# Kernel tuning notes

Measured on AMD Instinct MI355X. Metric: run time of the kernel, lower is better.

The kernel has to match this reference:

```python
import jax, jax.numpy as jnp
import numpy as np

D_MODEL = 1024
N_HEADS = 16
D_H = D_MODEL // N_HEADS
MAX_LEN = 2048
BATCH = 2
SEQ = 2048
EPS = 1e-8
W_SCALE = 0.02


def _rms_norm(x, w):
    # RMSNorm: x * rsqrt(mean(x^2) + eps) * w
    ms = jnp.mean(jnp.square(x), axis=-1, keepdims=True)
    return w * (x * jax.lax.rsqrt(ms + EPS))


def setup_inputs() -> dict:
    key = jax.random.key(0)
    ks = jax.random.split(key, 12)
    d = D_MODEL
    inp = {
        "x": jax.random.normal(ks[0], (BATCH, SEQ, d), dtype=jnp.float32),
        "t_bias": jnp.zeros((1,), dtype=jnp.float32),  # unused by the module
        "p_bias": jax.random.normal(ks[1], (MAX_LEN, N_HEADS), dtype=jnp.float32),
        # AMS layer params (Linear stored as [in, out])
        "wq": jax.random.normal(ks[2], (d, d), dtype=jnp.float32) * W_SCALE,
        "bq": jnp.zeros((d,), dtype=jnp.float32),
        "wk": jax.random.normal(ks[3], (d, d), dtype=jnp.float32) * W_SCALE,
        "bk": jnp.zeros((d,), dtype=jnp.float32),
        "wv": jax.random.normal(ks[4], (d, d), dtype=jnp.float32) * W_SCALE,
        "bv": jnp.zeros((d,), dtype=jnp.float32),
        "wu": jax.random.normal(ks[5], (d, d), dtype=jnp.float32) * W_SCALE,
        "bu": jnp.zeros((d,), dtype=jnp.float32),
        "g_ams": jnp.ones((d,), dtype=jnp.float32),   # shared RMSNorm weight in AMSLayer
        # MFFN layer params
        "w0": jax.random.normal(ks[6], (d, d), dtype=jnp.float32) * W_SCALE,
        "b0": jnp.zeros((d,), dtype=jnp.float32),
        "w1": jax.random.normal(ks[7], (d, 2 * d), dtype=jnp.float32) * W_SCALE,
        "b1": jnp.zeros((2 * d,), dtype=jnp.float32),
        "w2": jax.random.normal(ks[8], (d, d), dtype=jnp.float32) * W_SCALE,
        "b2": jnp.zeros((d,), dtype=jnp.float32),
        "g_mffn": jnp.ones((d,), dtype=jnp.float32),
    }
    return inp


def reference(x, t_bias, p_bias, wq, bq, wk, bk, wv, bv, wu, bu, g_ams,
              w0, b0, w1, b1, w2, b2, g_mffn):
    B, S, d = x.shape
    H, dh = N_HEADS, D_H

    # ---- AMS layer ----
    x_norm = _rms_norm(x, g_ams)

    def proj(w, b):
        # [B,S,d] -> [B,H,S,dh]
        return (x_norm @ w + b).reshape(B, S, H, dh).transpose(0, 2, 1, 3)

    q = proj(wq, bq)
    k = proj(wk, bk)
    v = proj(wv, bv)

    scale = 1.0 / np.sqrt(dh).astype(np.float32)
    score = jnp.einsum('bhsd,bhtd->bhst', q, k) * scale
    # additive positional bias: p_bias[:S].T -> [H,S], broadcast over query dim
    score = score + p_bias[:S, :].T[None, :, None, :]

    attn = jax.nn.silu(score)                        # SiLU instead of softmax
    out = jnp.einsum('bhst,bhtd->bhsd', attn, v)
    out = out.transpose(0, 2, 1, 3).reshape(B, S, d)

    u = jax.nn.silu(x_norm @ wu + bu)
    ams_out = _rms_norm(out, g_ams) * u

    # ---- MFFN layer ----
    o = (ams_out @ w0 + b0) + x
    o_norm = _rms_norm(o, g_mffn)
    x12 = o_norm @ w1 + b1
    x1, x2 = jnp.split(x12, 2, axis=-1)
    swiglu = jax.nn.silu(x1) * x2
    return (swiglu @ w2 + b2) + o
```

## Files before the change

### kernel.cpp

```cpp
#include <hip/hip_runtime.h>
#include <stdint.h>
#include <math.h>


#define D    1024
#define NH   16
#define DH   64
#define B_   2
#define S_   2048
#define ROWS 4096
#define LQ   4096
#define EPSR 1e-8f

typedef unsigned short u16;
typedef __attribute__((ext_vector_type(8))) short short8;
typedef __attribute__((ext_vector_type(4))) float f32x4;
typedef __attribute__((ext_vector_type(16))) float f32x16;
typedef __attribute__((ext_vector_type(4))) int int4v;

__device__ __forceinline__ float bf2f(u16 u) {
    union { uint32_t i; float f; } c; c.i = ((uint32_t)u) << 16; return c.f;
}
__device__ __forceinline__ u16 f2bf(float f) {
    union { float f; uint32_t i; } c; c.f = f;
    uint32_t x = c.i;
    x += 0x7fffu + ((x >> 16) & 1u);
    return (u16)(x >> 16);
}
#define LOG2E 1.44269504f
__device__ __forceinline__ float silu_fast(float v) {
    return v * __builtin_amdgcn_rcpf(1.0f + __builtin_amdgcn_exp2f(v * -LOG2E));
}

#define GLDS16(gp, lp) __builtin_amdgcn_global_load_lds( \
        (const __attribute__((address_space(1))) void*)(gp), \
        (__attribute__((address_space(3))) void*)(lp), 16, 0, 0)

__device__ __forceinline__ int xcd_work(int flat, int nwg) {
    return ((flat & 7) * (nwg >> 3)) + (flat >> 3);
}

__global__ __launch_bounds__(256) void transpose_all_kernel(
    const float* __restrict__ wq, const float* __restrict__ wk,
    const float* __restrict__ wv, const float* __restrict__ wu,
    const float* __restrict__ w0, const float* __restrict__ w2,
    const float* __restrict__ w1,
    u16* __restrict__ wT4, u16* __restrict__ w0T,
    u16* __restrict__ w2T, u16* __restrict__ w1T,
    const float* __restrict__ pb, float* __restrict__ pbT)
{
    const unsigned MI = 1u << 20;
    const int z = blockIdx.z;
    const int tid = threadIdx.x;
    if (z == 8) {
        if (blockIdx.y != 0) return;
        const int r = (blockIdx.x << 7) + (tid >> 1);
        const int c0 = (tid & 1) << 3;
        float4 v0 = *(const float4*)&pb[(size_t)r * NH + c0];
        float4 v1 = *(const float4*)&pb[(size_t)r * NH + c0 + 4];
        pbT[(size_t)(c0 + 0) * S_ + r] = v0.x;
        pbT[(size_t)(c0 + 1) * S_ + r] = v0.y;
        pbT[(size_t)(c0 + 2) * S_ + r] = v0.z;
        pbT[(size_t)(c0 + 3) * S_ + r] = v0.w;
        pbT[(size_t)(c0 + 4) * S_ + r] = v1.x;
        pbT[(size_t)(c0 + 5) * S_ + r] = v1.y;
        pbT[(size_t)(c0 + 6) * S_ + r] = v1.z;
        pbT[(size_t)(c0 + 7) * S_ + r] = v1.w;
        return;
    }
    const float* W; u16* WT; int N; int noff = 0;
    switch (z) {
        case 0: W = wq; WT = wT4;          N = 1024; break;
        case 1: W = wk; WT = wT4 + 1 * MI; N = 1024; break;
        case 2: W = wv; WT = wT4 + 2 * MI; N = 1024; break;
        case 3: W = wu; WT = wT4 + 3 * MI; N = 1024; break;
        case 4: W = w0; WT = w0T;          N = 1024; break;
        case 5: W = w2; WT = w2T;          N = 1024; break;
        case 6: W = w1; WT = w1T;          N = 2048; noff = 0;    break;
        default:W = w1; WT = w1T;          N = 2048; noff = 1024; break;
    }
    __shared__ float T[64][65];
    const int n0 = (blockIdx.x << 6) + noff;
    const int k0 = blockIdx.y << 6;
    const int rr = tid >> 4;
    const int cc = (tid & 15) << 2;
#pragma unroll
    for (int l = 0; l < 4; ++l) {
        const int r = rr + (l << 4);
        float4 v = *(const float4*)&W[(size_t)(k0 + r) * N + n0 + cc];
        T[cc + 0][r] = v.x; T[cc + 1][r] = v.y;
        T[cc + 2][r] = v.z; T[cc + 3][r] = v.w;
    }
    __syncthreads();
    const int n  = tid >> 2;
    const int ks = (tid & 3) << 4;
#pragma unroll
    for (int m = 0; m < 4; ++m) {
        const int k = ks + (m << 2);
        float4 v = *(const float4*)&T[n][k];
        ushort4 o;
        o.x = f2bf(v.x); o.y = f2bf(v.y); o.z = f2bf(v.z); o.w = f2bf(v.w);
        *(ushort4*)&WT[(size_t)(n0 + n) * 1024 + k0 + k] = o;
    }
}

__global__ __launch_bounds__(256) void rmsnorm_kernel(
    const float* __restrict__ inf, const u16* __restrict__ inb, int ldi,
    const float* __restrict__ g,
    const u16* __restrict__ mul, int ldm,
    u16* __restrict__ out, int ldo)
{
    const int row = blockIdx.x;
    const int tid = threadIdx.x;
    const int c = tid << 2;
    float x0, x1, x2, x3;
    if (inb) {
        ushort4 xi = *(const ushort4*)&inb[(size_t)row * ldi + c];
        x0 = bf2f(xi.x); x1 = bf2f(xi.y); x2 = bf2f(xi.z); x3 = bf2f(xi.w);
    } else {
        float4 xi = *(const float4*)&inf[(size_t)row * ldi + c];
        x0 = xi.x; x1 = xi.y; x2 = xi.z; x3 = xi.w;
    }
    float ss = x0*x0 + x1*x1 + x2*x2 + x3*x3;
#pragma unroll
    for (int off = 32; off > 0; off >>= 1) ss += __shfl_down(ss, off, 64);
    __shared__ float red[4];
    if ((tid & 63) == 0) red[tid >> 6] = ss;
    __syncthreads();
    float r = rsqrtf((red[0] + red[1] + red[2] + red[3]) * (1.0f / D) + EPSR);
    float4 gv = *(const float4*)&g[c];
    float v0 = x0 * r * gv.x, v1 = x1 * r * gv.y, v2 = x2 * r * gv.z, v3 = x3 * r * gv.w;
    if (mul) {
        ushort4 mi = *(const ushort4*)&mul[(size_t)row * ldm + c];
        v0 *= bf2f(mi.x); v1 *= bf2f(mi.y); v2 *= bf2f(mi.z); v3 *= bf2f(mi.w);
    }
    ushort4 o;
    o.x = f2bf(v0); o.y = f2bf(v1); o.z = f2bf(v2); o.w = f2bf(v3);
    *(ushort4*)&out[(size_t)row * ldo + c] = o;
}

__global__ __launch_bounds__(256) void gemm128(
    const u16* __restrict__ A, const u16* __restrict__ WT,
    const float* __restrict__ bs0, const float* __restrict__ bs1,
    const float* __restrict__ bs2, const float* __restrict__ bs3,
    u16* __restrict__ outb, int ldo, int actmask,
    u16* __restrict__ VT, int vtsel)
{
    __shared__ u16 As[128 * 64];
    __shared__ u16 Bs[128 * 64];
    const int tid  = threadIdx.x;
    const int wave = tid >> 6;
    const int lane = tid & 63;
    const int lm   = lane & 15;
    const int quad = lane >> 4;
    const int l7   = lm & 7;
    const int gx   = gridDim.x;
    const int gxm  = gx - 1;
    const int gxs  = __popc(gxm);
    const int work = xcd_work(blockIdx.x + (blockIdx.y << gxs), gx * gridDim.y);
    const int col0 = (work & gxm) << 7;
    const int row0 = (work >> gxs) << 7;
    const int wr = (wave >> 1) << 6;
    const int wc = (wave & 1) << 6;

    const int lr8  = lane >> 3;
    const int gch8 = ((lane & 7) ^ lr8) << 3;
    const u16* Ag = A  + (size_t)(row0 + wave * 32 + lr8) * 1024 + gch8;
    const u16* Bg = WT + (size_t)(col0 + wave * 32 + lr8) * 1024 + gch8;

    f32x4 acc[4][4] = {};

    for (int k0 = 0; k0 < 1024; k0 += 64) {
        __syncthreads();
#pragma unroll
        for (int j = 0; j < 4; ++j) {
            GLDS16(Ag + (size_t)(8 * j) * 1024 + k0, &As[(wave * 32 + 8 * j) * 64]);
            GLDS16(Bg + (size_t)(8 * j) * 1024 + k0, &Bs[(wave * 32 + 8 * j) * 64]);
        }
        __syncthreads();
#pragma unroll
        for (int kk = 0; kk < 2; ++kk) {
            short8 af[4], bf[4];
#pragma unroll
            for (int i = 0; i < 4; ++i)
                af[i] = *(const short8*)&As[(wr + i * 16 + lm) * 64 +
                                            (((kk * 4 + quad) ^ l7) << 3)];
#pragma unroll
            for (int j = 0; j < 4; ++j)
                bf[j] = *(const short8*)&Bs[(wc + j * 16 + lm) * 64 +
                                            (((kk * 4 + quad) ^ l7) << 3)];
#pragma unroll
            for (int i = 0; i < 4; ++i)
#pragma unroll
                for (int j = 0; j < 4; ++j)
                    acc[i][j] = __builtin_amdgcn_mfma_f32_16x16x32_bf16(af[i], bf[j], acc[i][j], 0, 0, 0);
        }
    }
    const int sel = col0 >> 10;
    const float* bias = (sel == 0) ? bs0 : (sel == 1) ? bs1 : (sel == 2) ? bs2 : bs3;
    const int act = (actmask >> sel) & 1;
    if (VT && sel == vtsel) {
        const int b = row0 >> 11;
#pragma unroll
        for (int j = 0; j < 4; ++j) {
            const int c2 = (col0 + wc + j * 16 + lm) & 1023;
            const int h  = c2 >> 6;
            const int dh = c2 & 63;
            const float bj = bias[c2];
            u16* vrow = VT + ((size_t)(b * NH + h) * 64 + dh) * (size_t)S_;
#pragma unroll
            for (int i = 0; i < 4; ++i) {
                const int tb = (row0 & 2047) + wr + i * 16 + quad * 4;
                ushort4 o;
                o.x = f2bf(acc[i][j][0] + bj);
                o.y = f2bf(acc[i][j][1] + bj);
                o.z = f2bf(acc[i][j][2] + bj);
                o.w = f2bf(acc[i][j][3] + bj);
                *(ushort4*)&vrow[tb] = o;
            }
        }
    } else {
#pragma unroll
        for (int j = 0; j < 4; ++j) {
            const int colg = col0 + wc + j * 16 + lm;
            const float bj = bias[colg & 1023];
#pragma unroll
            for (int i = 0; i < 4; ++i) {
#pragma unroll
                for (int r = 0; r < 4; ++r) {
                    const int rowg = row0 + wr + i * 16 + quad * 4 + r;
                    float v = acc[i][j][r] + bj;
                    if (act) v = silu_fast(v);
                    outb[(size_t)rowg * ldo + colg] = f2bf(v);
                }
            }
        }
    }
}

__global__ __launch_bounds__(256) void gemm64(
    const u16* __restrict__ A, int lda, const u16* __restrict__ WT,
    const float* __restrict__ bias,
    const float* __restrict__ res,
    float* __restrict__ outf, int ldo)
{
    __shared__ u16 As[64 * 64];
    __shared__ u16 Bs[64 * 64];
    const int tid  = threadIdx.x;
    const int wave = tid >> 6;
    const int lane = tid & 63;
    const int lm   = lane & 15;
    const int quad = lane >> 4;
    const int l7   = lm & 7;
    const int work = xcd_work(blockIdx.x + (blockIdx.y << 4), 1024);
    const int col0 = (work & 15) << 6;
    const int row0 = (work >> 4) << 6;
    const int wr = (wave >> 1) << 5;
    const int wc = (wave & 1) << 5;

    const int lr8  = lane >> 3;
    const int gch8 = ((lane & 7) ^ lr8) << 3;
    const u16* Ag = A  + (size_t)(row0 + wave * 16 + lr8) * lda + gch8;
    const u16* Bg = WT + (size_t)(col0 + wave * 16 + lr8) * 1024 + gch8;

    f32x4 acc[2][2] = {};

    for (int k0 = 0; k0 < 1024; k0 += 64) {
        __syncthreads();
        GLDS16(Ag + k0,                        &As[(wave * 16) * 64]);
        GLDS16(Ag + (size_t)8 * lda + k0,      &As[(wave * 16 + 8) * 64]);
        GLDS16(Bg + k0,                        &Bs[(wave * 16) * 64]);
        GLDS16(Bg + (size_t)8 * 1024 + k0,     &Bs[(wave * 16 + 8) * 64]);
        __syncthreads();
#pragma unroll
        for (int kk = 0; kk < 2; ++kk) {
            short8 af[2], bf[2];
#pragma unroll
            for (int i = 0; i < 2; ++i)
                af[i] = *(const short8*)&As[(wr + i * 16 + lm) * 64 +
                                            (((kk * 4 + quad) ^ l7) << 3)];
#pragma unroll
            for (int j = 0; j < 2; ++j)
                bf[j] = *(const short8*)&Bs[(wc + j * 16 + lm) * 64 +
                                            (((kk * 4 + quad) ^ l7) << 3)];
#pragma unroll
            for (int i = 0; i < 2; ++i)
#pragma unroll
                for (int j = 0; j < 2; ++j)
                    acc[i][j] = __builtin_amdgcn_mfma_f32_16x16x32_bf16(af[i], bf[j], acc[i][j], 0, 0, 0);
        }
    }
#pragma unroll
    for (int j = 0; j < 2; ++j) {
        const int colg = col0 + wc + j * 16 + lm;
        const float bj = bias[colg];
#pragma unroll
        for (int i = 0; i < 2; ++i) {
#pragma unroll
            for (int r = 0; r < 4; ++r) {
                const int rowg = row0 + wr + i * 16 + quad * 4 + r;
                const size_t idx = (size_t)rowg * ldo + colg;
                float v = acc[i][j][r] + bj;
                if (res) v += res[idx];
                outf[idx] = v;
            }
        }
    }
}

__global__ __launch_bounds__(256) void gemm_w1_swiglu(
    const u16* __restrict__ A, const u16* __restrict__ WT,
    const float* __restrict__ b1, u16* __restrict__ outb)
{
    __shared__ u16 As[64 * 64];
    __shared__ u16 Bs[128 * 64];
    const int tid  = threadIdx.x;
    const int wave = tid >> 6;
    const int lane = tid & 63;
    const int lm   = lane & 15;
    const int quad = lane >> 4;
    const int l7   = lm & 7;
    const int work = xcd_work(blockIdx.x + (blockIdx.y << 4), 1024);
    const int col0 = (work & 15) << 6;
    const int row0 = (work >> 4) << 6;
    const int wr  = (wave >> 1) << 5;
    const int wc2 = (wave & 1) << 5;

    const int lr8  = lane >> 3;
    const int gch8 = ((lane & 7) ^ lr8) << 3;
    const int sb   = wave * 32;
    const int brow = col0 + (sb & 63) + ((sb >> 6) << 10) + lr8;
    const u16* Ag = A  + (size_t)(row0 + wave * 16 + lr8) * 1024 + gch8;
    const u16* Bg = WT + (size_t)brow * 1024 + gch8;

    f32x4 acc[2][4] = {};

    for (int k0 = 0; k0 < 1024; k0 += 64) {
        __syncthreads();
        GLDS16(Ag + k0,                   &As[(wave * 16) * 64]);
        GLDS16(Ag + (size_t)8 * 1024 + k0,&As[(wave * 16 + 8) * 64]);
#pragma unroll
        for (int j = 0; j < 4; ++j)
            GLDS16(Bg + (size_t)(8 * j) * 1024 + k0, &Bs[(wave * 32 + 8 * j) * 64]);
        __syncthreads();
#pragma unroll
        for (int kk = 0; kk < 2; ++kk) {
            short8 af[2], bf[4];
#pragma unroll
            for (int i = 0; i < 2; ++i)
                af[i] = *(const short8*)&As[(wr + i * 16 + lm) * 64 +
                                            (((kk * 4 + quad) ^ l7) << 3)];
#pragma unroll
            for (int j = 0; j < 2; ++j) {
                bf[j]     = *(const short8*)&Bs[(wc2 + j * 16 + lm) * 64 +
                                                (((kk * 4 + quad) ^ l7) << 3)];
                bf[j + 2] = *(const short8*)&Bs[(64 + wc2 + j * 16 + lm) * 64 +
                                                (((kk * 4 + quad) ^ l7) << 3)];
            }
#pragma unroll
            for (int i = 0; i < 2; ++i)
#pragma unroll
                for (int j = 0; j < 4; ++j)
                    acc[i][j] = __builtin_amdgcn_mfma_f32_16x16x32_bf16(af[i], bf[j], acc[i][j], 0, 0, 0);
        }
    }
#pragma unroll
    for (int j = 0; j < 2; ++j) {
        const int colg = col0 + wc2 + j * 16 + lm;
        const float ba = b1[colg];
        const float bb = b1[1024 + colg];
#pragma unroll
        for (int i = 0; i < 2; ++i) {
#pragma unroll
            for (int r = 0; r < 4; ++r) {
                const int rowg = row0 + wr + i * 16 + quad * 4 + r;
                const float x1v = acc[i][j][r] + ba;
                const float x2v = acc[i][j + 2][r] + bb;
                outb[(size_t)rowg * LQ + colg] = f2bf(silu_fast(x1v) * x2v);
            }
        }
    }
}

__global__ __launch_bounds__(512, 2) void attn_mfma(
    const u16* __restrict__ qkvu, const u16* __restrict__ VT,
    const float* __restrict__ pbT, u16* __restrict__ out)
{
    __shared__ u16 Ks[2][2][64 * 64];
    __shared__ u16 Vs[2][2][64 * 64];
    __shared__ float pbl[S_];
    const int tid  = threadIdx.x;
    const int wave = tid >> 6;
    const int grp  = wave >> 2;
    const int wq4  = wave & 3;
    const int lane = tid & 63;
    const int l31  = lane & 31;
    const int hi   = lane >> 5;
    const int l7   = lane & 7;
    const int xorv = l7 ^ ((l31 >> 3) & 3);
    const int flat = blockIdx.x + (blockIdx.y << 4) + (blockIdx.z << 8);
    const int work = ((flat & 7) << 6) + (flat >> 3);
    const int s0 = (work & 15) << 7;
    const int h  = (work >> 4) & 15;
    const int b  = work >> 8;
    const size_t base = (size_t)b * S_ * LQ + (size_t)h * DH;
    const u16* q  = qkvu + base;
    const u16* kg = qkvu + base + 1024;
    const u16* vt = VT + (size_t)(b * NH + h) * 64 * S_;
    const float* pbh = pbT + (size_t)h * S_;

    for (int i = tid * 4; i < S_; i += 2048)
        *(float4*)&pbl[i] = *(const float4*)&pbh[i];

    const int qrow = s0 + wq4 * 32 + l31;
    short8 qf[4];
#pragma unroll
    for (int i = 0; i < 4; ++i)
        qf[i] = *(const short8*)&q[(size_t)qrow * LQ + i * 16 + hi * 8];

    const int lr  = lane >> 3;
    const int gA  = (2 * wq4) & 3;
    const int gB  = (2 * wq4 + 1) & 3;
    const u16* kgA = kg + (size_t)(16 * wq4 + lr) * LQ     + ((l7 ^ lr ^ gA) << 3);
    const u16* kgB = kg + (size_t)(16 * wq4 + 8 + lr) * LQ + ((l7 ^ lr ^ gB) << 3);
    const u16* vgA = vt + (size_t)(16 * wq4 + lr) * S_     + ((l7 ^ lr ^ gA) << 3);
    const u16* vgB = vt + (size_t)(16 * wq4 + 8 + lr) * S_ + ((l7 ^ lr ^ gB) << 3);

#define ISSUE(it, bu) do { \
        const size_t tn = ((size_t)(grp) * 16 + (size_t)(it)) << 6; \
        GLDS16(kgA + tn * LQ, &Ks[grp][bu][(16 * wq4) * 64]); \
        GLDS16(kgB + tn * LQ, &Ks[grp][bu][(16 * wq4 + 8) * 64]); \
        GLDS16(vgA + tn,      &Vs[grp][bu][(16 * wq4) * 64]); \
        GLDS16(vgB + tn,      &Vs[grp][bu][(16 * wq4 + 8) * 64]); \
    } while (0)

    f32x16 accO[2] = {};
    ISSUE(0, 0);
    __syncthreads();

#pragma unroll 1
    for (int it = 0; it < 16; ++it) {
        const int ib = it & 1;
        const int nb = ib ^ 1;
        if (it + 1 < 16) ISSUE(it + 1, nb);
        const int t0 = grp * 1024 + (it << 6);
        f32x16 st0 = {}, st1 = {};
        __builtin_amdgcn_s_setprio(1);
#pragma unroll
        for (int i = 0; i < 4; ++i) {
            const int co = ((2 * i + hi) ^ xorv) << 3;
            short8 kf0 = *(const short8*)&Ks[grp][ib][(l31) * 64 + co];
            short8 kf1 = *(const short8*)&Ks[grp][ib][(32 + l31) * 64 + co];
            st0 = __builtin_amdgcn_mfma_f32_32x32x16_bf16(kf0, qf[i], st0, 0, 0, 0);
            st1 = __builtin_amdgcn_mfma_f32_32x32x16_bf16(kf1, qf[i], st1, 0, 0, 0);
        }
        __builtin_amdgcn_s_setprio(0);
        int pk0[8], pk1[8];
#pragma unroll
        for (int g = 0; g < 4; ++g) {
            float4 pbv0 = *(const float4*)&pbl[t0 + 8 * g + 4 * hi];
            float4 pbv1 = *(const float4*)&pbl[t0 + 32 + 8 * g + 4 * hi];
            float a0 = silu_fast(fmaf(st0[4 * g + 0], 0.125f, pbv0.x));
            float a1 = silu_fast(fmaf(st0[4 * g + 1], 0.125f, pbv0.y));
            float a2 = silu_fast(fmaf(st0[4 * g + 2], 0.125f, pbv0.z));
            float a3 = silu_fast(fmaf(st0[4 * g + 3], 0.125f, pbv0.w));
            float b0 = silu_fast(fmaf(st1[4 * g + 0], 0.125f, pbv1.x));
            float b1 = silu_fast(fmaf(st1[4 * g + 1], 0.125f, pbv1.y));
            float b2 = silu_fast(fmaf(st1[4 * g + 2], 0.125f, pbv1.z));
            float b3 = silu_fast(fmaf(st1[4 * g + 3], 0.125f, pbv1.w));
            asm("v_cvt_pk_bf16_f32 %0, %1, %2" : "=v"(pk0[2 * g])     : "v"(a0), "v"(a1));
            asm("v_cvt_pk_bf16_f32 %0, %1, %2" : "=v"(pk0[2 * g + 1]) : "v"(a2), "v"(a3));
            asm("v_cvt_pk_bf16_f32 %0, %1, %2" : "=v"(pk1[2 * g])     : "v"(b0), "v"(b1));
            asm("v_cvt_pk_bf16_f32 %0, %1, %2" : "=v"(pk1[2 * g + 1]) : "v"(b2), "v"(b3));
        }
#pragma unroll
        for (int m = 0; m < 2; ++m) {
            int w0 = pk0[4 * m + 0], w2 = pk0[4 * m + 2];
            int w1 = pk0[4 * m + 1], w3 = pk0[4 * m + 3];
            asm("v_permlane32_swap_b32 %0, %1" : "+v"(w0), "+v"(w2));
            asm("v_permlane32_swap_b32 %0, %1" : "+v"(w1), "+v"(w3));
            int u0 = pk1[4 * m + 0], u2 = pk1[4 * m + 2];
            int u1 = pk1[4 * m + 1], u3 = pk1[4 * m + 3];
            asm("v_permlane32_swap_b32 %0, %1" : "+v"(u0), "+v"(u2));
            asm("v_permlane32_swap_b32 %0, %1" : "+v"(u1), "+v"(u3));
            union { int4v i; short8 s; } pa, pb2;
            pa.i.x  = w0; pa.i.y  = w1; pa.i.z  = w2; pa.i.w  = w3;
            pb2.i.x = u0; pb2.i.y = u1; pb2.i.z = u2; pb2.i.w = u3;
            __builtin_amdgcn_s_setprio(1);
#pragma unroll
            for (int n = 0; n < 2; ++n) {
                short8 vf0 = *(const short8*)&Vs[grp][ib][(32 * n + l31) * 64 +
                    (((2 * m + hi) ^ xorv) << 3)];
                short8 vf1 = *(const short8*)&Vs[grp][ib][(32 * n + l31) * 64 +
                    (((4 + 2 * m + hi) ^ xorv) << 3)];
                accO[n] = __builtin_amdgcn_mfma_f32_32x32x16_bf16(pa.s,  vf0, accO[n], 0, 0, 0);
                accO[n] = __builtin_amdgcn_mfma_f32_32x32x16_bf16(pb2.s, vf1, accO[n], 0, 0, 0);
            }
            __builtin_amdgcn_s_setprio(0);
        }
        __syncthreads();
    }
#undef ISSUE
    float* scr = (float*)&Ks[0][0][0];
    const int sl = wq4 * 64 + lane;
    if (grp == 1) {
#pragma unroll
        for (int n = 0; n < 2; ++n)
#pragma unroll
            for (int r = 0; r < 16; ++r)
                scr[(n * 16 + r) * 256 + sl] = accO[n][r];
    }
    __syncthreads();
    if (grp == 0) {
#pragma unroll
        for (int n = 0; n < 2; ++n)
#pragma unroll
            for (int r = 0; r < 16; ++r)
                accO[n][r] += scr[(n * 16 + r) * 256 + sl];
        const int qb = s0 + wq4 * 32 + 4 * hi;
#pragma unroll
        for (int n = 0; n < 2; ++n)
#pragma unroll
            for (int r = 0; r < 16; ++r) {
                const int qq = qb + (r & 3) + 8 * (r >> 2);
                out[base + (size_t)qq * LQ + 32 * n + l31] = f2bf(accO[n][r]);
            }
    }
}

extern "C" void kernel_launch(void* const* d_in, const int* in_sizes, int n_in,
                              void* d_out, int out_size, void* d_ws, size_t ws_size,
                              hipStream_t stream)
{
    const float* x      = (const float*)d_in[0];
    const float* pb     = (const float*)d_in[2];
    const float* wq     = (const float*)d_in[3];
    const float* bq     = (const float*)d_in[4];
    const float* wk     = (const float*)d_in[5];
    const float* bk     = (const float*)d_in[6];
    const float* wv     = (const float*)d_in[7];
    const float* bv     = (const float*)d_in[8];
    const float* wu     = (const float*)d_in[9];
    const float* bu     = (const float*)d_in[10];
    const float* g_ams  = (const float*)d_in[11];
    const float* w0     = (const float*)d_in[12];
    const float* b0     = (const float*)d_in[13];
    const float* w1     = (const float*)d_in[14];
    const float* b1     = (const float*)d_in[15];
    const float* w2     = (const float*)d_in[16];
    const float* b2     = (const float*)d_in[17];
    const float* g_mffn = (const float*)d_in[18];
    float* OUT = (float*)d_out;
    u16*   VT  = (u16*)d_out;
    float* pbT = (float*)((u16*)d_out + 4 * (1u << 20));

    const size_t MI = 1024 * 1024;
    u16* WS   = (u16*)d_ws;
    u16* wT4  = WS;
    u16* w0T  = WS + 4 * MI;
    u16* w2T  = WS + 5 * MI;
    u16* w1T  = WS + 6 * MI;
    u16* A0   = WS + 8 * MI;
    u16* QKVU = WS + 12 * MI;

    dim3 blk(256);

    transpose_all_kernel<<<dim3(16, 16, 9), blk, 0, stream>>>(
        wq, wk, wv, wu, w0, w2, w1, wT4, w0T, w2T, w1T, pb, pbT);

    rmsnorm_kernel<<<ROWS, blk, 0, stream>>>(x, nullptr, D, g_ams, nullptr, 0, A0, D);
    gemm128<<<dim3(32, 32), blk, 0, stream>>>(A0, wT4, bq, bk, bv, bu,
                                              QKVU, LQ, 0b1000, VT, 2);
    attn_mfma<<<dim3(16, 16, 2), dim3(512), 0, stream>>>(QKVU, VT, pbT, QKVU);
    rmsnorm_kernel<<<ROWS, blk, 0, stream>>>(nullptr, QKVU, LQ, g_ams, QKVU + 3072, LQ, A0, D);
    gemm64<<<dim3(16, 64), blk, 0, stream>>>(A0, D, w0T, b0, x, OUT, D);
    rmsnorm_kernel<<<ROWS, blk, 0, stream>>>(OUT, nullptr, D, g_mffn, nullptr, 0, A0, D);
    gemm_w1_swiglu<<<dim3(16, 64), blk, 0, stream>>>(A0, w1T, b1, QKVU + 2048);
    gemm64<<<dim3(16, 64), blk, 0, stream>>>(QKVU + 2048, LQ, w2T, b2, OUT, OUT, D);
    (void)ws_size; (void)in_sizes; (void)n_in; (void)out_size;
}
```

Before: 295.5 us.

## Fuse first RMSNorm into transpose launch and deepen gemm64 K tile

The standalone RMSNorm over the input is folded into the weight-transpose kernel as extra z-slices (z 9-24 cover 4096 rows), which removes one kernel launch and lets both run concurrently. Separately, gemm64 now stages a K tile of 128 instead of 64, with four 16-byte global-to-LDS loads per operand per wave. This halves the number of barrier pairs per tile at the cost of doubled LDS use per block. The swizzle is recomputed for the wider rows.

```diff
diff --git a/kernel.cpp b/kernel.cpp
--- a/kernel.cpp
+++ b/kernel.cpp
@@ -47,11 +47,32 @@
     const float* __restrict__ w1,
     u16* __restrict__ wT4, u16* __restrict__ w0T,
     u16* __restrict__ w2T, u16* __restrict__ w1T,
-    const float* __restrict__ pb, float* __restrict__ pbT)
+    const float* __restrict__ pb, float* __restrict__ pbT,
+    const float* __restrict__ xin, const float* __restrict__ g_ams,
+    u16* __restrict__ Aout)
 {
     const unsigned MI = 1u << 20;
     const int z = blockIdx.z;
     const int tid = threadIdx.x;
+    __shared__ float T[64][65];
+    __shared__ float red[4];
+    if (z >= 9) {
+        const int row = (z - 9) * 256 + blockIdx.y * 16 + blockIdx.x;
+        const int c = tid << 2;
+        float4 xi = *(const float4*)&xin[(size_t)row * D + c];
+        float ss = xi.x*xi.x + xi.y*xi.y + xi.z*xi.z + xi.w*xi.w;
+#pragma unroll
+        for (int off = 32; off > 0; off >>= 1) ss += __shfl_down(ss, off, 64);
+        if ((tid & 63) == 0) red[tid >> 6] = ss;
+        __syncthreads();
+        float r = rsqrtf((red[0] + red[1] + red[2] + red[3]) * (1.0f / D) + EPSR);
+        float4 gv = *(const float4*)&g_ams[c];
+        ushort4 o;
+        o.x = f2bf(xi.x * r * gv.x); o.y = f2bf(xi.y * r * gv.y);
+        o.z = f2bf(xi.z * r * gv.z); o.w = f2bf(xi.w * r * gv.w);
+        *(ushort4*)&Aout[(size_t)row * D + c] = o;
+        return;
+    }
     if (z == 8) {
         if (blockIdx.y != 0) return;
         const int r = (blockIdx.x << 7) + (tid >> 1);
@@ -79,7 +100,6 @@
         case 6: W = w1; WT = w1T;          N = 2048; noff = 0;    break;
         default:W = w1; WT = w1T;          N = 2048; noff = 1024; break;
     }
-    __shared__ float T[64][65];
     const int n0 = (blockIdx.x << 6) + noff;
     const int k0 = blockIdx.y << 6;
     const int rr = tid >> 4;
@@ -244,8 +264,8 @@
     const float* __restrict__ res,
     float* __restrict__ outf, int ldo)
 {
-    __shared__ u16 As[64 * 64];
-    __shared__ u16 Bs[64 * 64];
+    __shared__ u16 As[64 * 128];
+    __shared__ u16 Bs[64 * 128];
     const int tid  = threadIdx.x;
     const int wave = tid >> 6;
     const int lane = tid & 63;
@@ -258,30 +278,38 @@
     const int wr = (wave >> 1) << 5;
     const int wc = (wave & 1) << 5;
 
-    const int lr8  = lane >> 3;
-    const int gch8 = ((lane & 7) ^ lr8) << 3;
-    const u16* Ag = A  + (size_t)(row0 + wave * 16 + lr8) * lda + gch8;
-    const u16* Bg = WT + (size_t)(col0 + wave * 16 + lr8) * 1024 + gch8;
+    const int l4  = lane >> 4;
+    const int c16 = lane & 15;
+    const u16* AgJ[4];
+    const u16* BgJ[4];
+#pragma unroll
+    for (int j = 0; j < 4; ++j) {
+        const int ro = 4 * j + l4;
+        const int gc = (c16 ^ (ro & 7)) << 3;
+        AgJ[j] = A  + (size_t)(row0 + wave * 16 + ro) * lda + gc;
+        BgJ[j] = WT + (size_t)(col0 + wave * 16 + ro) * 1024 + gc;
+    }
 
     f32x4 acc[2][2] = {};
 
-    for (int k0 = 0; k0 < 1024; k0 += 64) {
-        __syncthreads();
-        GLDS16(Ag + k0,                        &As[(wave * 16) * 64]);
-        GLDS16(Ag + (size_t)8 * lda + k0,      &As[(wave * 16 + 8) * 64]);
-        GLDS16(Bg + k0,                        &Bs[(wave * 16) * 64]);
-        GLDS16(Bg + (size_t)8 * 1024 + k0,     &Bs[(wave * 16 + 8) * 64]);
-        __syncthreads();
-#pragma unroll
-        for (int kk = 0; kk < 2; ++kk) {
+    for (int k0 = 0; k0 < 1024; k0 += 128) {
+        __syncthreads();
+#pragma unroll
+        for (int j = 0; j < 4; ++j) {
+            GLDS16(AgJ[j] + k0, &As[(wave * 16 + 4 * j) * 128]);
+            GLDS16(BgJ[j] + k0, &Bs[(wave * 16 + 4 * j) * 128]);
+        }
+        __syncthreads();
+#pragma unroll
+        for (int kk = 0; kk < 4; ++kk) {
             short8 af[2], bf[2];
 #pragma unroll
             for (int i = 0; i < 2; ++i)
-                af[i] = *(const short8*)&As[(wr + i * 16 + lm) * 64 +
+                af[i] = *(const short8*)&As[(wr + i * 16 + lm) * 128 +
                                             (((kk * 4 + quad) ^ l7) << 3)];
 #pragma unroll
             for (int j = 0; j < 2; ++j)
-                bf[j] = *(const short8*)&Bs[(wc + j * 16 + lm) * 64 +
+                bf[j] = *(const short8*)&Bs[(wc + j * 16 + lm) * 128 +
                                             (((kk * 4 + quad) ^ l7) << 3)];
 #pragma unroll
             for (int i = 0; i < 2; ++i)
@@ -565,10 +593,9 @@
 
     dim3 blk(256);
 
-    transpose_all_kernel<<<dim3(16, 16, 9), blk, 0, stream>>>(
-        wq, wk, wv, wu, w0, w2, w1, wT4, w0T, w2T, w1T, pb, pbT);
-
-    rmsnorm_kernel<<<ROWS, blk, 0, stream>>>(x, nullptr, D, g_ams, nullptr, 0, A0, D);
+    transpose_all_kernel<<<dim3(16, 16, 25), blk, 0, stream>>>(
+        wq, wk, wv, wu, w0, w2, w1, wT4, w0T, w2T, w1T, pb, pbT, x, g_ams, A0);
+
     gemm128<<<dim3(32, 32), blk, 0, stream>>>(A0, wT4, bq, bk, bv, bu,
                                               QKVU, LQ, 0b1000, VT, 2);
     attn_mfma<<<dim3(16, 16, 2), dim3(512), 0, stream>>>(QKVU, VT, pbT, QKVU);
```

After: 299.7 us. About the same (+1.4%).
